# Kernel optimization log

Hardware: AMD Instinct MI355X
Metric: run time of the kernel (lower is better)

Reference implementation:

```python
import jax, jax.numpy as jnp
import numpy as np

EMBED_DIM = 1024
N_HEADS = 16
HEAD_DIM = EMBED_DIM // N_HEADS
B, S = 2, 2048


def setup_inputs() -> dict:
    key = jax.random.key(0)
    ks = jax.random.split(key, 7)
    scale = 1.0 / np.sqrt(EMBED_DIM)
    return {
        "query": jax.random.normal(ks[0], (B, S, EMBED_DIM), dtype=jnp.float32),
        "key": jax.random.normal(ks[1], (B, S, EMBED_DIM), dtype=jnp.float32),
        "value": jax.random.normal(ks[2], (B, S, EMBED_DIM), dtype=jnp.float32),
        # nn.Linear weights stored as [out, in]; y = x @ W.T
        "Wq": jax.random.normal(ks[3], (EMBED_DIM, EMBED_DIM), dtype=jnp.float32) * scale,
        "Wk": jax.random.normal(ks[4], (EMBED_DIM, EMBED_DIM), dtype=jnp.float32) * scale,
        "Wv": jax.random.normal(ks[5], (EMBED_DIM, EMBED_DIM), dtype=jnp.float32) * scale,
        "Wo": jax.random.normal(ks[6], (EMBED_DIM, EMBED_DIM), dtype=jnp.float32) * scale,
    }


def reference(query, key, value, Wq, Wk, Wv, Wo):
    # Projections (Linear, no bias): x @ W.T
    Q = query @ Wq.T  # [B, S, E]
    K = key @ Wk.T
    V = value @ Wv.T
    b, s, _ = Q.shape
    # Split heads: slicing head i of [..., E] == reshape to [B, S, H, D]
    Qh = Q.reshape(b, s, N_HEADS, HEAD_DIM)
    Kh = K.reshape(b, s, N_HEADS, HEAD_DIM)
    Vh = V.reshape(b, s, N_HEADS, HEAD_DIM)
    scores = jnp.einsum("bqhd,bkhd->bhqk", Qh, Kh) / jnp.sqrt(
        jnp.asarray(HEAD_DIM, dtype=Qh.dtype)
    )  # [B, H, Sq, Sk]
    attn = jax.nn.softmax(scores, axis=-1)
    out = jnp.einsum("bhqk,bkhd->bqhd", attn, Vh)  # [B, Sq, H, D]
    out = out.reshape(b, s, N_HEADS * HEAD_DIM)  # concat heads
    return out @ Wo.T
```

## Files before the change

### kernel.cpp

```cpp
#include <hip/hip_runtime.h>
#include <hip/hip_bf16.h>
#include <stdint.h>
#include <stddef.h>

#define EMBED 1024
#define NHEAD 16
#define HDIM  64
#define BATCH 2
#define SEQ   2048
#define MTOT  (BATCH*SEQ)

typedef __hip_bfloat16 bf16;
typedef __attribute__((ext_vector_type(8))) __bf16 bf16x8;
typedef __attribute__((ext_vector_type(4))) float  f32x4;
typedef __attribute__((ext_vector_type(16))) float f32x16;

#define GLD16(gp, lp) __builtin_amdgcn_global_load_lds( \
    (__attribute__((address_space(1))) void*)(gp),      \
    (__attribute__((address_space(3))) void*)(lp), 16, 0, 0)


__device__ __forceinline__ ushort4 cvt4(const float4 v) {
  union { ushort4 u; bf16 b[4]; } o;
  o.b[0] = __float2bfloat16(v.x);
  o.b[1] = __float2bfloat16(v.y);
  o.b[2] = __float2bfloat16(v.z);
  o.b[3] = __float2bfloat16(v.w);
  return o.u;
}

__device__ __forceinline__ uint32_t pk2(float lo, float hi) {
  union { bf16 h[2]; uint32_t u; } r;
  r.h[0] = __float2bfloat16(lo);
  r.h[1] = __float2bfloat16(hi);
  return r.u;
}

__device__ __forceinline__ bool detect_bf16(const uint32_t* __restrict__ x, int t) {
  uint32_t w = x[(size_t)(t & 63) * 997u];
  int e = (int)((w >> 7) & 0xFF);
  unsigned long long m = __ballot(e >= 100 && e <= 135);
  return __popcll(m) >= 48;
}

#define SM_C1 0.18033688011112042f
#define SM_C0 -14.426950408889634f

__global__ __launch_bounds__(256)
void convert_inputs(const void* xs0, const void* xs1, const void* xs2,
                    const void* ws0, const void* ws1, const void* ws2, const void* ws3,
                    bf16* __restrict__ xd0, bf16* __restrict__ xd1, bf16* __restrict__ xd2,
                    bf16* __restrict__ wd0, bf16* __restrict__ wd1,
                    bf16* __restrict__ wd2, bf16* __restrict__ wd3) {
  const int bid = blockIdx.x;
  const void* src; bf16* dst; size_t base;
  if (bid < 6144) {
    const int a = bid >> 11;
    src = a == 0 ? xs0 : a == 1 ? xs1 : xs2;
    dst = a == 0 ? xd0 : a == 1 ? xd1 : xd2;
    base = (size_t)(bid & 2047) * 2048;
  } else {
    const int a = (bid - 6144) >> 9;
    src = a == 0 ? ws0 : a == 1 ? ws1 : a == 2 ? ws2 : ws3;
    dst = a == 0 ? wd0 : a == 1 ? wd1 : a == 2 ? wd2 : wd3;
    base = (size_t)((bid - 6144) & 511) * 2048;
  }
  const bool isbf = detect_bf16((const uint32_t*)src, threadIdx.x);
  const size_t off = base + (size_t)threadIdx.x * 8;
  if (isbf) {
    *(uint4*)((ushort*)dst + off) = *(const uint4*)((const ushort*)src + off);
  } else {
    const float* s = (const float*)src + off;
    float4 a4 = *(const float4*)(s);
    float4 b4 = *(const float4*)(s + 4);
    *(ushort4*)((ushort*)dst + off)     = cvt4(a4);
    *(ushort4*)((ushort*)dst + off + 4) = cvt4(b4);
  }
}

template<int TM, int TN>
__device__ __forceinline__ void gemm_nt_dbuf(
    const bf16* __restrict__ X, const bf16* __restrict__ W,
    bf16* sA, bf16* sB, f32x4 (&acc)[TM/32][TN/32],
    int row0, int col0, int t, int wr, int wc, int l16, int quad,
    int k0, int klen) {
  constexpr int CA = TM / 32, CB = TN / 32;
  constexpr int RI = TM / 32, RJ = TN / 32;
  constexpr int PF  = CA + CB;
  const int nit = klen >> 6;

  const bf16* gA[CA]; const bf16* gB[CB];
  int la[CA], lb[CB];
#pragma unroll
  for (int c = 0; c < CA; ++c) {
    int id = c * 256 + t, r = id >> 3;
    int cc = (((id & 7) ^ (r & 7)) * 8);
    gA[c] = X + (size_t)(row0 + r) * EMBED + k0 + cc;  la[c] = id * 8;
  }
#pragma unroll
  for (int c = 0; c < CB; ++c) {
    int id = c * 256 + t, r = id >> 3;
    int cc = (((id & 7) ^ (r & 7)) * 8);
    gB[c] = W + (size_t)(col0 + r) * EMBED + k0 + cc;  lb[c] = id * 8;
  }

  auto issue = [&](int kb, int buf) {
#pragma unroll
    for (int c = 0; c < CA; ++c) GLD16(gA[c] + kb, sA + buf * (TM * 64) + la[c]);
#pragma unroll
    for (int c = 0; c < CB; ++c) GLD16(gB[c] + kb, sB + buf * (TN * 64) + lb[c]);
  };
  const int xr = l16 & 7;
  auto compute = [&](int buf) {
    const bf16* pA = sA + buf * (TM * 64);
    const bf16* pB = sB + buf * (TN * 64);
#pragma unroll
    for (int kk = 0; kk < 64; kk += 32) {
      const int ch = (kk >> 3) + quad;
      bf16x8 a[RI], b[RJ];
#pragma unroll
      for (int i = 0; i < RI; ++i)
        a[i] = *(const bf16x8*)(pA + (wr + 16 * i + l16) * 64 + ((ch ^ xr) << 3));
#pragma unroll
      for (int j = 0; j < RJ; ++j)
        b[j] = *(const bf16x8*)(pB + (wc + 16 * j + l16) * 64 + ((ch ^ xr) << 3));
#pragma unroll
      for (int i = 0; i < RI; ++i)
#pragma unroll
        for (int j = 0; j < RJ; ++j)
          acc[i][j] = __builtin_amdgcn_mfma_f32_16x16x32_bf16(a[i], b[j], acc[i][j], 0, 0, 0);
    }
  };

  issue(0, 0);
  int p = 0;
  for (int i = 0; i < nit - 1; ++i) {
    issue((i + 1) * 64, p ^ 1);
    asm volatile("s_waitcnt vmcnt(%0)\ns_barrier" :: "i"(PF) : "memory");
    compute(p);
    asm volatile("s_barrier" ::: "memory");
    p ^= 1;
  }
  asm volatile("s_waitcnt vmcnt(0)\ns_barrier" ::: "memory");
  compute(p);
}

template<int TM, int TN, bool ABF, bool BBF>
__device__ __forceinline__ void gemm_nt_slow(
    const void* __restrict__ X, const void* __restrict__ W,
    bf16* sA, bf16* sB, f32x4 (&acc)[TM/32][TN/32],
    int row0, int col0, int t, int wr, int wc, int l16, int quad,
    int k0, int klen) {
  constexpr int RI = TM / 32, RJ = TN / 32;
  const int xr = l16 & 7;
  for (int kb = k0; kb < k0 + klen; kb += 64) {
    if constexpr (ABF) {
      const bf16* s = (const bf16*)X;
#pragma unroll
      for (int c = 0; c < TM / 32; ++c) {
        int id = c * 256 + t, r = id >> 3;
        int cc = (((id & 7) ^ (r & 7)) * 8);
        GLD16(s + (size_t)(row0 + r) * EMBED + kb + cc, sA + id * 8);
      }
    } else {
      const float* s = (const float*)X;
#pragma unroll
      for (int c = 0; c < TM / 16; ++c) {
        int id = c * 256 + t, r = id >> 4;
        int lc = (id & 15) >> 1, half = (id & 1) * 4;
        float4 v = *(const float4*)(s + (size_t)(row0 + r) * EMBED + kb + lc * 8 + half);
        *(ushort4*)(sA + r * 64 + ((lc ^ (r & 7)) << 3) + half) = cvt4(v);
      }
    }
    if constexpr (BBF) {
      const bf16* s = (const bf16*)W;
#pragma unroll
      for (int c = 0; c < TN / 32; ++c) {
        int id = c * 256 + t, r = id >> 3;
        int cc = (((id & 7) ^ (r & 7)) * 8);
        GLD16(s + (size_t)(col0 + r) * EMBED + kb + cc, sB + id * 8);
      }
    } else {
      const float* s = (const float*)W;
#pragma unroll
      for (int c = 0; c < TN / 16; ++c) {
        int id = c * 256 + t, r = id >> 4;
        int lc = (id & 15) >> 1, half = (id & 1) * 4;
        float4 v = *(const float4*)(s + (size_t)(col0 + r) * EMBED + kb + lc * 8 + half);
        *(ushort4*)(sB + r * 64 + ((lc ^ (r & 7)) << 3) + half) = cvt4(v);
      }
    }
    __syncthreads();
#pragma unroll
    for (int kk = 0; kk < 64; kk += 32) {
      const int ch = (kk >> 3) + quad;
      bf16x8 a[RI], b[RJ];
#pragma unroll
      for (int i = 0; i < RI; ++i)
        a[i] = *(const bf16x8*)(sA + (wr + 16 * i + l16) * 64 + ((ch ^ xr) << 3));
#pragma unroll
      for (int j = 0; j < RJ; ++j)
        b[j] = *(const bf16x8*)(sB + (wc + 16 * j + l16) * 64 + ((ch ^ xr) << 3));
#pragma unroll
      for (int i = 0; i < RI; ++i)
#pragma unroll
        for (int j = 0; j < RJ; ++j)
          acc[i][j] = __builtin_amdgcn_mfma_f32_16x16x32_bf16(a[i], b[j], acc[i][j], 0, 0, 0);
    }
    __syncthreads();
  }
}

__global__ __launch_bounds__(256, 2)
void qkv_proj_kernel(const void* Xq, const void* Xk, const void* Xv,
                     const void* Wq, const void* Wk, const void* Wv,
                     bf16* __restrict__ Qo, bf16* __restrict__ Ko,
                     bf16* __restrict__ Vto) {
  __shared__ __align__(16) bf16 sA[2 * 128 * 64];
  __shared__ __align__(16) bf16 sB[2 * 128 * 64];
  const int t    = threadIdx.x;
  const int wave = t >> 6, lane = t & 63;
  const int quad = lane >> 4, l16 = lane & 15;
  const int wr = (wave & 1) * 64;
  const int wc = (wave >> 1) * 64;
  const bool isbf = detect_bf16((const uint32_t*)Xq, t);

  for (int ti = blockIdx.x; ti < 768; ti += 512) {
    const int sel  = ti >> 8;
    const int col0 = ((ti >> 5) & 7) * 128;
    const int row0 = (ti & 31) * 128;
    const void* X = (sel == 0) ? Xq : (sel == 1) ? Xk : Xv;
    const void* W = (sel == 0) ? Wq : (sel == 1) ? Wk : Wv;

    f32x4 acc[4][4] = {};
    if (isbf)
      gemm_nt_dbuf<128, 128>((const bf16*)X, (const bf16*)W, sA, sB, acc,
                             row0, col0, t, wr, wc, l16, quad, 0, EMBED);
    else
      gemm_nt_slow<128, 128, false, false>(X, W, sA, sB, acc,
                                           row0, col0, t, wr, wc, l16, quad, 0, EMBED);

    if (sel < 2) {
      bf16* C = (sel == 0) ? Qo : Ko;
      const float sc = (sel == 0) ? SM_C1 : 1.0f;
#pragma unroll
      for (int i = 0; i < 4; ++i)
#pragma unroll
        for (int j = 0; j < 4; ++j)
#pragma unroll
          for (int r = 0; r < 4; ++r) {
            int m = row0 + wr + 16 * i + quad * 4 + r;
            int n = col0 + wc + 16 * j + l16;
            C[(size_t)m * EMBED + n] = __float2bfloat16(acc[i][j][r] * sc);
          }
    } else {
#pragma unroll
      for (int i = 0; i < 4; ++i)
#pragma unroll
        for (int j = 0; j < 4; ++j)
#pragma unroll
          for (int r = 0; r < 4; ++r) {
            int m = row0 + wr + 16 * i + quad * 4 + r;
            int n = col0 + wc + 16 * j + l16;
            int b = m >> 11, s = m & (SEQ - 1);
            int h = n >> 6,  d = n & (HDIM - 1);
            Vto[(((size_t)(b * NHEAD + h)) * HDIM + d) * SEQ + s] =
                __float2bfloat16(acc[i][j][r]);
          }
    }
    __syncthreads();
  }
}

__global__ __launch_bounds__(256, 2)
void out_proj_partial(const bf16* __restrict__ X, const void* W,
                      const uint32_t* __restrict__ qref, float* __restrict__ P) {
  __shared__ __align__(16) bf16 sA[2 * 128 * 64];
  __shared__ __align__(16) bf16 sB[2 * 128 * 64];
  const int t    = threadIdx.x;
  const int wave = t >> 6, lane = t & 63;
  const int quad = lane >> 4, l16 = lane & 15;
  const int row0 = blockIdx.x * 128;
  const int col0 = blockIdx.y * 128;
  const int z    = blockIdx.z;
  const int wr = (wave & 1) * 64;
  const int wc = (wave >> 1) * 64;
  const bool isbf = detect_bf16(qref, t);

  f32x4 acc[4][4] = {};
  if (isbf)
    gemm_nt_dbuf<128, 128>(X, (const bf16*)W, sA, sB, acc,
                           row0, col0, t, wr, wc, l16, quad, z * 512, 512);
  else
    gemm_nt_slow<128, 128, true, false>(X, W, sA, sB, acc,
                                        row0, col0, t, wr, wc, l16, quad, z * 512, 512);

  float* Pz = P + (size_t)z * MTOT * EMBED;
#pragma unroll
  for (int i = 0; i < 4; ++i)
#pragma unroll
    for (int j = 0; j < 4; ++j)
#pragma unroll
      for (int r = 0; r < 4; ++r) {
        int m = row0 + wr + 16 * i + quad * 4 + r;
        int n = col0 + wc + 16 * j + l16;
        Pz[(size_t)m * EMBED + n] = acc[i][j][r];
      }
}

__global__ __launch_bounds__(256)
void reduce_splitk(const float* __restrict__ P,
                   const uint32_t* __restrict__ qref, void* __restrict__ C) {
  const bool isbf = detect_bf16(qref, threadIdx.x);
  size_t i = ((size_t)blockIdx.x * 256 + threadIdx.x) * 4;
  float4 a = *(const float4*)(P + i);
  float4 b = *(const float4*)(P + (size_t)MTOT * EMBED + i);
  float4 s = make_float4(a.x + b.x, a.y + b.y, a.z + b.z, a.w + b.w);
  if (isbf) *(ushort4*)((bf16*)C + i) = cvt4(s);
  else      *(float4*)((float*)C + i) = s;
}

__global__ __launch_bounds__(256, 2)
void out_proj_kernel(const bf16* __restrict__ X, const void* W,
                     const uint32_t* __restrict__ qref, void* C) {
  __shared__ __align__(16) bf16 sA[2 * 64 * 64];
  __shared__ __align__(16) bf16 sB[2 * 128 * 64];
  const int t    = threadIdx.x;
  const int wave = t >> 6, lane = t & 63;
  const int quad = lane >> 4, l16 = lane & 15;
  const int row0 = blockIdx.x * 64;
  const int col0 = blockIdx.y * 128;
  const int wr = (wave & 1) * 32;
  const int wc = (wave >> 1) * 64;
  const bool isbf = detect_bf16(qref, t);

  f32x4 acc[2][4] = {};
  if (isbf)
    gemm_nt_dbuf<64, 128>(X, (const bf16*)W, sA, sB, acc,
                          row0, col0, t, wr, wc, l16, quad, 0, EMBED);
  else
    gemm_nt_slow<64, 128, true, false>(X, W, sA, sB, acc,
                                       row0, col0, t, wr, wc, l16, quad, 0, EMBED);

#pragma unroll
  for (int i = 0; i < 2; ++i)
#pragma unroll
    for (int j = 0; j < 4; ++j)
#pragma unroll
      for (int r = 0; r < 4; ++r) {
        int m = row0 + wr + 16 * i + quad * 4 + r;
        int n = col0 + wc + 16 * j + l16;
        if (isbf)
          ((bf16*)C)[(size_t)m * EMBED + n] = __float2bfloat16(acc[i][j][r]);
        else
          ((float*)C)[(size_t)m * EMBED + n] = acc[i][j][r];
      }
}

__global__ __launch_bounds__(256, 2)
void flash_kernel(const bf16* __restrict__ Q, const bf16* __restrict__ K,
                  const bf16* __restrict__ Vt, bf16* __restrict__ O) {
  __shared__ __align__(16) bf16 sK[2][64 * 64];
  __shared__ __align__(16) bf16 sV[2][64 * 64];

  const int t    = threadIdx.x;
  const int wave = t >> 6, lane = t & 63;
  const int l5 = lane & 31, hi = lane >> 5;
  const int x5 = l5 & 7;

  const int L  = ((blockIdx.x & 7) << 6) + (blockIdx.x >> 3);
  const int qt = L & 15;
  const int h  = (L >> 4) & 15;
  const int b  = L >> 8;
  const int qw = qt * 128 + 32 * wave;

  const bf16* Kg = K + ((size_t)b * SEQ) * EMBED + h * HDIM;
  const bf16* Vg = Vt + (((size_t)(b * NHEAD + h)) * HDIM) * SEQ;

  bf16x8 aq[4];
  {
    const bf16* Qrow = Q + ((size_t)b * SEQ + qw + l5) * EMBED + h * HDIM + hi * 8;
#pragma unroll
    for (int g = 0; g < 4; ++g) aq[g] = *(const bf16x8*)(Qrow + 16 * g);
  }

  union { bf16x8 v; bf16 e[8]; } ones;
#pragma unroll
  for (int i = 0; i < 8; ++i) ones.e[i] = __float2bfloat16(1.0f);

  auto issueK = [&](int kt, int buf) {
#pragma unroll
    for (int c = 0; c < 2; ++c) {
      int id = c * 256 + t, r = id >> 3;
      int cc = (((id & 7) ^ (r & 7)) * 8);
      GLD16(Kg + (size_t)(kt + r) * EMBED + cc, &sK[buf][id * 8]);
    }
  };
  auto issueV = [&](int kt, int buf) {
#pragma unroll
    for (int c = 0; c < 2; ++c) {
      int id = c * 256 + t, r = id >> 3;
      int cc = (((id & 7) ^ (r & 7)) * 8);
      GLD16(Vg + (size_t)r * SEQ + kt + cc, &sV[buf][id * 8]);
    }
  };

  f32x16 o0 = {}, o1 = {};
  f32x16 ls = {};
  f32x16 pT0, pT1;

  auto qk = [&](int buf, f32x16& T0, f32x16& T1) {
#pragma unroll
    for (int r = 0; r < 16; ++r) { T0[r] = SM_C0; T1[r] = SM_C0; }
    __builtin_amdgcn_s_setprio(1);
#pragma unroll
    for (int g = 0; g < 4; ++g) {
      const int ch = 2 * g + hi;
      bf16x8 ak0 = *(const bf16x8*)(&sK[buf][(l5)      * 64 + ((ch ^ x5) << 3)]);
      bf16x8 ak1 = *(const bf16x8*)(&sK[buf][(32 + l5) * 64 + ((ch ^ x5) << 3)]);
      T0 = __builtin_amdgcn_mfma_f32_32x32x16_bf16(ak0, aq[g], T0, 0, 0, 0);
      T1 = __builtin_amdgcn_mfma_f32_32x32x16_bf16(ak1, aq[g], T1, 0, 0, 0);
    }
    __builtin_amdgcn_s_setprio(0);
  };

  auto smax = [&](const f32x16& T0, const f32x16& T1, bf16x8 (&PA)[4]) {
#pragma unroll
    for (int kg = 0; kg < 2; ++kg) {
      float p[16];
#pragma unroll
      for (int r = 0; r < 16; ++r)
        p[r] = __builtin_amdgcn_exp2f(kg ? T1[r] : T0[r]);
#pragma unroll
      for (int s = 0; s < 2; ++s) {
        uint32_t c0 = pk2(p[8 * s + 0], p[8 * s + 1]);
        uint32_t c1 = pk2(p[8 * s + 2], p[8 * s + 3]);
        uint32_t c2 = pk2(p[8 * s + 4], p[8 * s + 5]);
        uint32_t c3 = pk2(p[8 * s + 6], p[8 * s + 7]);
        uint32_t x = __shfl_xor(hi ? c0 : c2, 32, 64);
        uint32_t y = __shfl_xor(hi ? c1 : c3, 32, 64);
        union { uint32_t u[4]; bf16x8 v; } w;
        w.u[0] = hi ? x  : c0;
        w.u[1] = hi ? y  : c1;
        w.u[2] = hi ? c2 : x;
        w.u[3] = hi ? c3 : y;
        PA[2 * kg + s] = w.v;
      }
    }
  };

  auto pv = [&](const bf16x8 (&PA)[4], int buf) {
    __builtin_amdgcn_s_setprio(1);
#pragma unroll
    for (int kk = 0; kk < 4; ++kk) {
      const int ch = 2 * kk + hi;
      ls = __builtin_amdgcn_mfma_f32_32x32x16_bf16(PA[kk], ones.v, ls, 0, 0, 0);
      bf16x8 bv0 = *(const bf16x8*)(&sV[buf][(l5)      * 64 + ((ch ^ x5) << 3)]);
      bf16x8 bv1 = *(const bf16x8*)(&sV[buf][(32 + l5) * 64 + ((ch ^ x5) << 3)]);
      o0 = __builtin_amdgcn_mfma_f32_32x32x16_bf16(PA[kk], bv0, o0, 0, 0, 0);
      o1 = __builtin_amdgcn_mfma_f32_32x32x16_bf16(PA[kk], bv1, o1, 0, 0, 0);
    }
    __builtin_amdgcn_s_setprio(0);
  };

  issueK(0, 0); issueV(0, 0); issueK(64, 1);
  asm volatile("s_waitcnt vmcnt(2)\ns_barrier" ::: "memory");
  qk(0, pT0, pT1);
  asm volatile("s_barrier" ::: "memory");

#pragma unroll 2
  for (int i = 0; i < SEQ / 64 - 1; ++i) {
    issueK((i + 2) * 64, i & 1);
    issueV((i + 1) * 64, (i + 1) & 1);
    asm volatile("s_waitcnt vmcnt(4)\ns_barrier" ::: "memory");
    f32x16 nT0, nT1;
    qk((i + 1) & 1, nT0, nT1);
    bf16x8 PA[4];
    smax(pT0, pT1, PA);
    pv(PA, i & 1);
    asm volatile("s_barrier" ::: "memory");
    pT0 = nT0; pT1 = nT1;
  }

  asm volatile("s_waitcnt vmcnt(0)\ns_barrier" ::: "memory");
  {
    bf16x8 PA[4];
    smax(pT0, pT1, PA);
    pv(PA, (SEQ / 64 - 1) & 1);
  }

  bf16* Og = O + ((size_t)b * SEQ + qw) * EMBED + h * HDIM + l5;
#pragma unroll
  for (int r = 0; r < 16; ++r) {
    const int m = (r & 3) + 8 * (r >> 2) + 4 * hi;
    const float inv = 1.0f / ls[r];
    Og[(size_t)m * EMBED]      = __float2bfloat16(o0[r] * inv);
    Og[(size_t)m * EMBED + 32] = __float2bfloat16(o1[r] * inv);
  }
}

extern "C" void kernel_launch(void* const* d_in, const int* in_sizes, int n_in,
                              void* d_out, int out_size, void* d_ws, size_t ws_size,
                              hipStream_t stream) {
  (void)in_sizes; (void)n_in; (void)out_size;
  bf16* Qp  = (bf16*)((char*)d_ws + 256);
  bf16* Kp  = Qp  + (size_t)MTOT * EMBED;
  bf16* Vtp = Kp  + (size_t)MTOT * EMBED;
  bf16* Op  = Vtp + (size_t)MTOT * EMBED;
  float* Pf = (float*)(Op + (size_t)MTOT * EMBED);

  bf16* Xqb = (bf16*)Pf;
  bf16* Xkb = Xqb + (size_t)MTOT * EMBED;
  bf16* Xvb = Xkb + (size_t)MTOT * EMBED;
  bf16* Wqb = Xvb + (size_t)MTOT * EMBED;
  bf16* Wkb = Wqb + (size_t)EMBED * EMBED;
  bf16* Wvb = Wkb + (size_t)EMBED * EMBED;
  bf16* Wob = (bf16*)((char*)Pf + (size_t)2 * MTOT * EMBED * 4);

  const size_t need_split = 256 + (size_t)MTOT * EMBED * 2 * 4
                          + (size_t)MTOT * EMBED * 4 * 2;
  const size_t need_conv  = need_split + (size_t)EMBED * EMBED * 2;

  if (ws_size >= need_conv) {
    convert_inputs<<<dim3(8192), 256, 0, stream>>>(
        d_in[0], d_in[1], d_in[2], d_in[3], d_in[4], d_in[5], d_in[6],
        Xqb, Xkb, Xvb, Wqb, Wkb, Wvb, Wob);
    qkv_proj_kernel<<<dim3(512), 256, 0, stream>>>(
        Xqb, Xkb, Xvb, Wqb, Wkb, Wvb, Qp, Kp, Vtp);
    flash_kernel<<<dim3(512), 256, 0, stream>>>(Qp, Kp, Vtp, Op);
    out_proj_partial<<<dim3(32, 8, 2), 256, 0, stream>>>(
        Op, Wob, (const uint32_t*)Qp, Pf);
    reduce_splitk<<<dim3(MTOT * EMBED / 1024), 256, 0, stream>>>(
        Pf, (const uint32_t*)d_in[0], d_out);
  } else if (ws_size >= need_split) {
    qkv_proj_kernel<<<dim3(512), 256, 0, stream>>>(
        d_in[0], d_in[1], d_in[2], d_in[3], d_in[4], d_in[5], Qp, Kp, Vtp);
    flash_kernel<<<dim3(512), 256, 0, stream>>>(Qp, Kp, Vtp, Op);
    out_proj_partial<<<dim3(32, 8, 2), 256, 0, stream>>>(
        Op, d_in[6], (const uint32_t*)d_in[0], Pf);
    reduce_splitk<<<dim3(MTOT * EMBED / 1024), 256, 0, stream>>>(
        Pf, (const uint32_t*)d_in[0], d_out);
  } else {
    qkv_proj_kernel<<<dim3(512), 256, 0, stream>>>(
        d_in[0], d_in[1], d_in[2], d_in[3], d_in[4], d_in[5], Qp, Kp, Vtp);
    flash_kernel<<<dim3(512), 256, 0, stream>>>(Qp, Kp, Vtp, Op);
    out_proj_kernel<<<dim3(64, 8), 256, 0, stream>>>(
        Op, d_in[6], (const uint32_t*)d_in[0], d_out);
  }
}
```

Before: 216.9 us.

## Split flash attention over two KV halves with a combine kernel

The flash attention kernel is templated so that, in the default workspace path, each (batch, head, query-tile) is split into two blocks that each process half of the key/value sequence. The grid doubles to 1024 blocks and the occupancy hint rises to four blocks per CU. Unnormalized fp32 partial outputs and row sums go to workspace, and a new reduce kernel adds the two halves, normalizes and converts to bf16. This aims to raise parallelism and latency hiding on the GPU. In exchange it adds an extra launch, fp32 partial-output traffic and possible register pressure from the tighter launch bound. Summing the halves directly is only correct if the softmax uses a fixed reference rather than a per-half running max.

```diff
diff --git a/kernel.cpp b/kernel.cpp
--- a/kernel.cpp
+++ b/kernel.cpp
@@ -357,9 +357,11 @@
       }
 }
 
-__global__ __launch_bounds__(256, 2)
+template<bool SPLIT>
+__global__ __launch_bounds__(256, SPLIT ? 4 : 2)
 void flash_kernel(const bf16* __restrict__ Q, const bf16* __restrict__ K,
-                  const bf16* __restrict__ Vt, bf16* __restrict__ O) {
+                  const bf16* __restrict__ Vt, bf16* __restrict__ O,
+                  float* __restrict__ Po, float* __restrict__ Ls) {
   __shared__ __align__(16) bf16 sK[2][64 * 64];
   __shared__ __align__(16) bf16 sV[2][64 * 64];
 
@@ -368,10 +370,14 @@
   const int l5 = lane & 31, hi = lane >> 5;
   const int x5 = l5 & 7;
 
-  const int L  = ((blockIdx.x & 7) << 6) + (blockIdx.x >> 3);
+  constexpr int LSH = SPLIT ? 7 : 6;
+  const int L  = ((blockIdx.x & 7) << LSH) | (blockIdx.x >> 3);
   const int qt = L & 15;
   const int h  = (L >> 4) & 15;
-  const int b  = L >> 8;
+  const int b  = (L >> 8) & 1;
+  const int z  = SPLIT ? (L >> 9) : 0;
+  constexpr int HT = SPLIT ? 16 : 32;
+  const int k0 = z << 10;
   const int qw = qt * 128 + 32 * wave;
 
   const bf16* Kg = K + ((size_t)b * SEQ) * EMBED + h * HDIM;
@@ -463,15 +469,15 @@
     __builtin_amdgcn_s_setprio(0);
   };
 
-  issueK(0, 0); issueV(0, 0); issueK(64, 1);
+  issueK(k0, 0); issueV(k0, 0); issueK(k0 + 64, 1);
   asm volatile("s_waitcnt vmcnt(2)\ns_barrier" ::: "memory");
   qk(0, pT0, pT1);
   asm volatile("s_barrier" ::: "memory");
 
 #pragma unroll 2
-  for (int i = 0; i < SEQ / 64 - 1; ++i) {
-    issueK((i + 2) * 64, i & 1);
-    issueV((i + 1) * 64, (i + 1) & 1);
+  for (int i = 0; i < HT - 1; ++i) {
+    issueK(k0 + (i + 2) * 64, i & 1);
+    issueV(k0 + (i + 1) * 64, (i + 1) & 1);
     asm volatile("s_waitcnt vmcnt(4)\ns_barrier" ::: "memory");
     f32x16 nT0, nT1;
     qk((i + 1) & 1, nT0, nT1);
@@ -486,17 +492,50 @@
   {
     bf16x8 PA[4];
     smax(pT0, pT1, PA);
-    pv(PA, (SEQ / 64 - 1) & 1);
-  }
-
-  bf16* Og = O + ((size_t)b * SEQ + qw) * EMBED + h * HDIM + l5;
-#pragma unroll
-  for (int r = 0; r < 16; ++r) {
-    const int m = (r & 3) + 8 * (r >> 2) + 4 * hi;
-    const float inv = 1.0f / ls[r];
-    Og[(size_t)m * EMBED]      = __float2bfloat16(o0[r] * inv);
-    Og[(size_t)m * EMBED + 32] = __float2bfloat16(o1[r] * inv);
-  }
+    pv(PA, (HT - 1) & 1);
+  }
+
+  if constexpr (SPLIT) {
+    float* Pg = Po + ((size_t)z * MTOT + b * SEQ + qw) * EMBED + h * HDIM + l5;
+#pragma unroll
+    for (int r = 0; r < 16; ++r) {
+      const int m = (r & 3) + 8 * (r >> 2) + 4 * hi;
+      Pg[(size_t)m * EMBED]      = o0[r];
+      Pg[(size_t)m * EMBED + 32] = o1[r];
+    }
+    if (l5 == 0) {
+      float* Lp = Ls + ((size_t)z * MTOT + b * SEQ + qw) * NHEAD + h;
+#pragma unroll
+      for (int r = 0; r < 16; ++r) {
+        const int m = (r & 3) + 8 * (r >> 2) + 4 * hi;
+        Lp[(size_t)m * NHEAD] = ls[r];
+      }
+    }
+  } else {
+    bf16* Og = O + ((size_t)b * SEQ + qw) * EMBED + h * HDIM + l5;
+#pragma unroll
+    for (int r = 0; r < 16; ++r) {
+      const int m = (r & 3) + 8 * (r >> 2) + 4 * hi;
+      const float inv = 1.0f / ls[r];
+      Og[(size_t)m * EMBED]      = __float2bfloat16(o0[r] * inv);
+      Og[(size_t)m * EMBED + 32] = __float2bfloat16(o1[r] * inv);
+    }
+  }
+}
+
+__global__ __launch_bounds__(256)
+void flash_reduce(const float* __restrict__ Po, const float* __restrict__ Ls,
+                  bf16* __restrict__ O) {
+  size_t i = ((size_t)blockIdx.x * 256 + threadIdx.x) * 4;
+  const size_t m = i >> 10;
+  const int h = (int)((i >> 6) & 15);
+  float4 a = *(const float4*)(Po + i);
+  float4 c = *(const float4*)(Po + (size_t)MTOT * EMBED + i);
+  float l0 = Ls[m * NHEAD + h];
+  float l1 = Ls[(size_t)MTOT * NHEAD + m * NHEAD + h];
+  float inv = 1.0f / (l0 + l1);
+  *(ushort4*)(O + i) = cvt4(make_float4((a.x + c.x) * inv, (a.y + c.y) * inv,
+                                        (a.z + c.z) * inv, (a.w + c.w) * inv));
 }
 
 extern "C" void kernel_launch(void* const* d_in, const int* in_sizes, int n_in,
@@ -516,10 +555,12 @@
   bf16* Wkb = Wqb + (size_t)EMBED * EMBED;
   bf16* Wvb = Wkb + (size_t)EMBED * EMBED;
   bf16* Wob = (bf16*)((char*)Pf + (size_t)2 * MTOT * EMBED * 4);
+  float* Lsp = (float*)(Wob + (size_t)EMBED * EMBED);
 
   const size_t need_split = 256 + (size_t)MTOT * EMBED * 2 * 4
                           + (size_t)MTOT * EMBED * 4 * 2;
-  const size_t need_conv  = need_split + (size_t)EMBED * EMBED * 2;
+  const size_t need_conv  = need_split + (size_t)EMBED * EMBED * 2
+                          + (size_t)2 * MTOT * NHEAD * 4;
 
   if (ws_size >= need_conv) {
     convert_inputs<<<dim3(8192), 256, 0, stream>>>(
@@ -527,7 +568,9 @@
         Xqb, Xkb, Xvb, Wqb, Wkb, Wvb, Wob);
     qkv_proj_kernel<<<dim3(512), 256, 0, stream>>>(
         Xqb, Xkb, Xvb, Wqb, Wkb, Wvb, Qp, Kp, Vtp);
-    flash_kernel<<<dim3(512), 256, 0, stream>>>(Qp, Kp, Vtp, Op);
+    flash_kernel<true><<<dim3(1024), 256, 0, stream>>>(
+        Qp, Kp, Vtp, Op, Pf, Lsp);
+    flash_reduce<<<dim3(MTOT * EMBED / 1024), 256, 0, stream>>>(Pf, Lsp, Op);
     out_proj_partial<<<dim3(32, 8, 2), 256, 0, stream>>>(
         Op, Wob, (const uint32_t*)Qp, Pf);
     reduce_splitk<<<dim3(MTOT * EMBED / 1024), 256, 0, stream>>>(
@@ -535,7 +578,8 @@
   } else if (ws_size >= need_split) {
     qkv_proj_kernel<<<dim3(512), 256, 0, stream>>>(
         d_in[0], d_in[1], d_in[2], d_in[3], d_in[4], d_in[5], Qp, Kp, Vtp);
-    flash_kernel<<<dim3(512), 256, 0, stream>>>(Qp, Kp, Vtp, Op);
+    flash_kernel<false><<<dim3(512), 256, 0, stream>>>(
+        Qp, Kp, Vtp, Op, Pf, (float*)Pf);
     out_proj_partial<<<dim3(32, 8, 2), 256, 0, stream>>>(
         Op, d_in[6], (const uint32_t*)d_in[0], Pf);
     reduce_splitk<<<dim3(MTOT * EMBED / 1024), 256, 0, stream>>>(
@@ -543,7 +587,8 @@
   } else {
     qkv_proj_kernel<<<dim3(512), 256, 0, stream>>>(
         d_in[0], d_in[1], d_in[2], d_in[3], d_in[4], d_in[5], Qp, Kp, Vtp);
-    flash_kernel<<<dim3(512), 256, 0, stream>>>(Qp, Kp, Vtp, Op);
+    flash_kernel<false><<<dim3(512), 256, 0, stream>>>(
+        Qp, Kp, Vtp, Op, Pf, (float*)Pf);
     out_proj_kernel<<<dim3(64, 8), 256, 0, stream>>>(
         Op, d_in[6], (const uint32_t*)d_in[0], d_out);
   }
```

Measured after the change: 458.8 us. 111% more time.

## Split key sequence across two wave groups in flash kernel and merge via LDS

Applied to the files above, without the earlier changes.

Doubles the flash kernel block to 512 threads. Each half of the waves processes half of the key/value sequence with its own double-buffered LDS tiles. The partial output and row sums from the second half are written to LDS and added by the first half before normalization and store. This shortens the serial per-block KV loop and raises waves per CU, at the cost of doubled LDS usage, an extra reduction epilogue, and possible register pressure.

```diff
diff --git a/kernel.cpp b/kernel.cpp
--- a/kernel.cpp
+++ b/kernel.cpp
@@ -357,22 +357,27 @@
       }
 }
 
-__global__ __launch_bounds__(256, 2)
+__global__ __launch_bounds__(512, 2)
 void flash_kernel(const bf16* __restrict__ Q, const bf16* __restrict__ K,
                   const bf16* __restrict__ Vt, bf16* __restrict__ O) {
-  __shared__ __align__(16) bf16 sK[2][64 * 64];
-  __shared__ __align__(16) bf16 sV[2][64 * 64];
+  __shared__ __align__(16) bf16 sK[2][2][64 * 64];
+  __shared__ __align__(16) bf16 sV[2][2][64 * 64];
 
   const int t    = threadIdx.x;
   const int wave = t >> 6, lane = t & 63;
   const int l5 = lane & 31, hi = lane >> 5;
   const int x5 = l5 & 7;
-
-  const int L  = ((blockIdx.x & 7) << 6) + (blockIdx.x >> 3);
+  const int z  = wave >> 2;
+  const int wq = wave & 3;
+  const int ct = t & 255;
+  const int k0 = z << 10;
+  constexpr int HT = 16;
+
+  const int L  = ((blockIdx.x & 7) << 6) | (blockIdx.x >> 3);
   const int qt = L & 15;
   const int h  = (L >> 4) & 15;
   const int b  = L >> 8;
-  const int qw = qt * 128 + 32 * wave;
+  const int qw = qt * 128 + 32 * wq;
 
   const bf16* Kg = K + ((size_t)b * SEQ) * EMBED + h * HDIM;
   const bf16* Vg = Vt + (((size_t)(b * NHEAD + h)) * HDIM) * SEQ;
@@ -391,17 +396,17 @@
   auto issueK = [&](int kt, int buf) {
 #pragma unroll
     for (int c = 0; c < 2; ++c) {
-      int id = c * 256 + t, r = id >> 3;
+      int id = c * 256 + ct, r = id >> 3;
       int cc = (((id & 7) ^ (r & 7)) * 8);
-      GLD16(Kg + (size_t)(kt + r) * EMBED + cc, &sK[buf][id * 8]);
+      GLD16(Kg + (size_t)(kt + r) * EMBED + cc, &sK[buf][z][id * 8]);
     }
   };
   auto issueV = [&](int kt, int buf) {
 #pragma unroll
     for (int c = 0; c < 2; ++c) {
-      int id = c * 256 + t, r = id >> 3;
+      int id = c * 256 + ct, r = id >> 3;
       int cc = (((id & 7) ^ (r & 7)) * 8);
-      GLD16(Vg + (size_t)r * SEQ + kt + cc, &sV[buf][id * 8]);
+      GLD16(Vg + (size_t)r * SEQ + kt + cc, &sV[buf][z][id * 8]);
     }
   };
 
@@ -416,8 +421,8 @@
 #pragma unroll
     for (int g = 0; g < 4; ++g) {
       const int ch = 2 * g + hi;
-      bf16x8 ak0 = *(const bf16x8*)(&sK[buf][(l5)      * 64 + ((ch ^ x5) << 3)]);
-      bf16x8 ak1 = *(const bf16x8*)(&sK[buf][(32 + l5) * 64 + ((ch ^ x5) << 3)]);
+      bf16x8 ak0 = *(const bf16x8*)(&sK[buf][z][(l5)      * 64 + ((ch ^ x5) << 3)]);
+      bf16x8 ak1 = *(const bf16x8*)(&sK[buf][z][(32 + l5) * 64 + ((ch ^ x5) << 3)]);
       T0 = __builtin_amdgcn_mfma_f32_32x32x16_bf16(ak0, aq[g], T0, 0, 0, 0);
       T1 = __builtin_amdgcn_mfma_f32_32x32x16_bf16(ak1, aq[g], T1, 0, 0, 0);
     }
@@ -455,23 +460,23 @@
     for (int kk = 0; kk < 4; ++kk) {
       const int ch = 2 * kk + hi;
       ls = __builtin_amdgcn_mfma_f32_32x32x16_bf16(PA[kk], ones.v, ls, 0, 0, 0);
-      bf16x8 bv0 = *(const bf16x8*)(&sV[buf][(l5)      * 64 + ((ch ^ x5) << 3)]);
-      bf16x8 bv1 = *(const bf16x8*)(&sV[buf][(32 + l5) * 64 + ((ch ^ x5) << 3)]);
+      bf16x8 bv0 = *(const bf16x8*)(&sV[buf][z][(l5)      * 64 + ((ch ^ x5) << 3)]);
+      bf16x8 bv1 = *(const bf16x8*)(&sV[buf][z][(32 + l5) * 64 + ((ch ^ x5) << 3)]);
       o0 = __builtin_amdgcn_mfma_f32_32x32x16_bf16(PA[kk], bv0, o0, 0, 0, 0);
       o1 = __builtin_amdgcn_mfma_f32_32x32x16_bf16(PA[kk], bv1, o1, 0, 0, 0);
     }
     __builtin_amdgcn_s_setprio(0);
   };
 
-  issueK(0, 0); issueV(0, 0); issueK(64, 1);
+  issueK(k0, 0); issueV(k0, 0); issueK(k0 + 64, 1);
   asm volatile("s_waitcnt vmcnt(2)\ns_barrier" ::: "memory");
   qk(0, pT0, pT1);
   asm volatile("s_barrier" ::: "memory");
 
 #pragma unroll 2
-  for (int i = 0; i < SEQ / 64 - 1; ++i) {
-    issueK((i + 2) * 64, i & 1);
-    issueV((i + 1) * 64, (i + 1) & 1);
+  for (int i = 0; i < HT - 1; ++i) {
+    issueK(k0 + (i + 2) * 64, i & 1);
+    issueV(k0 + (i + 1) * 64, (i + 1) & 1);
     asm volatile("s_waitcnt vmcnt(4)\ns_barrier" ::: "memory");
     f32x16 nT0, nT1;
     qk((i + 1) & 1, nT0, nT1);
@@ -486,16 +491,33 @@
   {
     bf16x8 PA[4];
     smax(pT0, pT1, PA);
-    pv(PA, (SEQ / 64 - 1) & 1);
-  }
-
-  bf16* Og = O + ((size_t)b * SEQ + qw) * EMBED + h * HDIM + l5;
-#pragma unroll
-  for (int r = 0; r < 16; ++r) {
-    const int m = (r & 3) + 8 * (r >> 2) + 4 * hi;
-    const float inv = 1.0f / ls[r];
-    Og[(size_t)m * EMBED]      = __float2bfloat16(o0[r] * inv);
-    Og[(size_t)m * EMBED + 32] = __float2bfloat16(o1[r] * inv);
+    pv(PA, (HT - 1) & 1);
+  }
+
+  float* sO = (float*)&sK[0][0][0];
+  float* sL = (float*)&sV[0][0][0];
+  __syncthreads();
+  if (z == 1) {
+#pragma unroll
+    for (int r = 0; r < 16; ++r) {
+      const int m = (r & 3) + 8 * (r >> 2) + 4 * hi;
+      sO[(32 * wq + m) * 64 + l5]      = o0[r];
+      sO[(32 * wq + m) * 64 + l5 + 32] = o1[r];
+      if (l5 == 0) sL[32 * wq + m] = ls[r];
+    }
+  }
+  __syncthreads();
+  if (z == 0) {
+    bf16* Og = O + ((size_t)b * SEQ + qw) * EMBED + h * HDIM + l5;
+#pragma unroll
+    for (int r = 0; r < 16; ++r) {
+      const int m = (r & 3) + 8 * (r >> 2) + 4 * hi;
+      const float inv = 1.0f / (ls[r] + sL[32 * wq + m]);
+      Og[(size_t)m * EMBED] =
+          __float2bfloat16((o0[r] + sO[(32 * wq + m) * 64 + l5]) * inv);
+      Og[(size_t)m * EMBED + 32] =
+          __float2bfloat16((o1[r] + sO[(32 * wq + m) * 64 + l5 + 32]) * inv);
+    }
   }
 }
 
@@ -527,7 +549,7 @@
         Xqb, Xkb, Xvb, Wqb, Wkb, Wvb, Wob);
     qkv_proj_kernel<<<dim3(512), 256, 0, stream>>>(
         Xqb, Xkb, Xvb, Wqb, Wkb, Wvb, Qp, Kp, Vtp);
-    flash_kernel<<<dim3(512), 256, 0, stream>>>(Qp, Kp, Vtp, Op);
+    flash_kernel<<<dim3(512), 512, 0, stream>>>(Qp, Kp, Vtp, Op);
     out_proj_partial<<<dim3(32, 8, 2), 256, 0, stream>>>(
         Op, Wob, (const uint32_t*)Qp, Pf);
     reduce_splitk<<<dim3(MTOT * EMBED / 1024), 256, 0, stream>>>(
@@ -535,7 +557,7 @@
   } else if (ws_size >= need_split) {
     qkv_proj_kernel<<<dim3(512), 256, 0, stream>>>(
         d_in[0], d_in[1], d_in[2], d_in[3], d_in[4], d_in[5], Qp, Kp, Vtp);
-    flash_kernel<<<dim3(512), 256, 0, stream>>>(Qp, Kp, Vtp, Op);
+    flash_kernel<<<dim3(512), 512, 0, stream>>>(Qp, Kp, Vtp, Op);
     out_proj_partial<<<dim3(32, 8, 2), 256, 0, stream>>>(
         Op, d_in[6], (const uint32_t*)d_in[0], Pf);
     reduce_splitk<<<dim3(MTOT * EMBED / 1024), 256, 0, stream>>>(
@@ -543,7 +565,7 @@
   } else {
     qkv_proj_kernel<<<dim3(512), 256, 0, stream>>>(
         d_in[0], d_in[1], d_in[2], d_in[3], d_in[4], d_in[5], Qp, Kp, Vtp);
-    flash_kernel<<<dim3(512), 256, 0, stream>>>(Qp, Kp, Vtp, Op);
+    flash_kernel<<<dim3(512), 512, 0, stream>>>(Qp, Kp, Vtp, Op);
     out_proj_kernel<<<dim3(64, 8), 256, 0, stream>>>(
         Op, d_in[6], (const uint32_t*)d_in[0], d_out);
   }
```

After: 226.8 us. 1.05x slower.

## Rebalance QKV projection tiles across blocks and use permlane32 swap in softmax

Applied to the files above, without the earlier changes.

The QKV projection kernel previously had 512 blocks loop over 768 128x128 tiles, so some blocks ran two tiles and others one. Now each block computes one Q or K 128x128 tile and then one 64x128 half-tile of V, which evens out the per-block work. In the flash kernel, the ds_bpermute-based shfl_xor plus selects that exchange bf16 halves across 32-lane halves are replaced with the gfx950 permlane32_swap intrinsic. The rebalancing adds a second GEMM prologue per block and uses smaller V tiles with less reuse.

```diff
diff --git a/kernel.cpp b/kernel.cpp
--- a/kernel.cpp
+++ b/kernel.cpp
@@ -221,16 +221,16 @@
   const int t    = threadIdx.x;
   const int wave = t >> 6, lane = t & 63;
   const int quad = lane >> 4, l16 = lane & 15;
-  const int wr = (wave & 1) * 64;
   const int wc = (wave >> 1) * 64;
   const bool isbf = detect_bf16((const uint32_t*)Xq, t);
 
-  for (int ti = blockIdx.x; ti < 768; ti += 512) {
-    const int sel  = ti >> 8;
-    const int col0 = ((ti >> 5) & 7) * 128;
-    const int row0 = (ti & 31) * 128;
-    const void* X = (sel == 0) ? Xq : (sel == 1) ? Xk : Xv;
-    const void* W = (sel == 0) ? Wq : (sel == 1) ? Wk : Wv;
+  {
+    const int sel  = blockIdx.x >> 8;
+    const int col0 = ((blockIdx.x >> 5) & 7) * 128;
+    const int row0 = (blockIdx.x & 31) * 128;
+    const void* X = sel ? Xk : Xq;
+    const void* W = sel ? Wk : Wq;
+    const int wr = (wave & 1) * 64;
 
     f32x4 acc[4][4] = {};
     if (isbf)
@@ -240,35 +240,49 @@
       gemm_nt_slow<128, 128, false, false>(X, W, sA, sB, acc,
                                            row0, col0, t, wr, wc, l16, quad, 0, EMBED);
 
-    if (sel < 2) {
-      bf16* C = (sel == 0) ? Qo : Ko;
-      const float sc = (sel == 0) ? SM_C1 : 1.0f;
-#pragma unroll
-      for (int i = 0; i < 4; ++i)
-#pragma unroll
-        for (int j = 0; j < 4; ++j)
-#pragma unroll
-          for (int r = 0; r < 4; ++r) {
-            int m = row0 + wr + 16 * i + quad * 4 + r;
-            int n = col0 + wc + 16 * j + l16;
-            C[(size_t)m * EMBED + n] = __float2bfloat16(acc[i][j][r] * sc);
-          }
-    } else {
-#pragma unroll
-      for (int i = 0; i < 4; ++i)
-#pragma unroll
-        for (int j = 0; j < 4; ++j)
-#pragma unroll
-          for (int r = 0; r < 4; ++r) {
-            int m = row0 + wr + 16 * i + quad * 4 + r;
-            int n = col0 + wc + 16 * j + l16;
-            int b = m >> 11, s = m & (SEQ - 1);
-            int h = n >> 6,  d = n & (HDIM - 1);
-            Vto[(((size_t)(b * NHEAD + h)) * HDIM + d) * SEQ + s] =
-                __float2bfloat16(acc[i][j][r]);
-          }
-    }
-    __syncthreads();
+    bf16* C = sel ? Ko : Qo;
+    const float sc = sel ? 1.0f : SM_C1;
+#pragma unroll
+    for (int i = 0; i < 4; ++i)
+#pragma unroll
+      for (int j = 0; j < 4; ++j)
+#pragma unroll
+        for (int r = 0; r < 4; ++r) {
+          int m = row0 + wr + 16 * i + quad * 4 + r;
+          int n = col0 + wc + 16 * j + l16;
+          C[(size_t)m * EMBED + n] = __float2bfloat16(acc[i][j][r] * sc);
+        }
+  }
+  __syncthreads();
+
+  {
+    const int tt   = blockIdx.x >> 1;
+    const int half = blockIdx.x & 1;
+    const int col0 = ((tt >> 5) & 7) * 128;
+    const int row0 = (tt & 31) * 128 + half * 64;
+    const int wr = (wave & 1) * 32;
+
+    f32x4 acc[2][4] = {};
+    if (isbf)
+      gemm_nt_dbuf<64, 128>((const bf16*)Xv, (const bf16*)Wv, sA, sB, acc,
+                            row0, col0, t, wr, wc, l16, quad, 0, EMBED);
+    else
+      gemm_nt_slow<64, 128, false, false>(Xv, Wv, sA, sB, acc,
+                                          row0, col0, t, wr, wc, l16, quad, 0, EMBED);
+
+#pragma unroll
+    for (int i = 0; i < 2; ++i)
+#pragma unroll
+      for (int j = 0; j < 4; ++j)
+#pragma unroll
+        for (int r = 0; r < 4; ++r) {
+          int m = row0 + wr + 16 * i + quad * 4 + r;
+          int n = col0 + wc + 16 * j + l16;
+          int b = m >> 11, s = m & (SEQ - 1);
+          int h = n >> 6,  d = n & (HDIM - 1);
+          Vto[(((size_t)(b * NHEAD + h)) * HDIM + d) * SEQ + s] =
+              __float2bfloat16(acc[i][j][r]);
+        }
   }
 }
 
@@ -368,7 +382,7 @@
   const int l5 = lane & 31, hi = lane >> 5;
   const int x5 = l5 & 7;
 
-  const int L  = ((blockIdx.x & 7) << 6) + (blockIdx.x >> 3);
+  const int L  = ((blockIdx.x & 7) << 6) | (blockIdx.x >> 3);
   const int qt = L & 15;
   const int h  = (L >> 4) & 15;
   const int b  = L >> 8;
@@ -437,13 +451,13 @@
         uint32_t c1 = pk2(p[8 * s + 2], p[8 * s + 3]);
         uint32_t c2 = pk2(p[8 * s + 4], p[8 * s + 5]);
         uint32_t c3 = pk2(p[8 * s + 6], p[8 * s + 7]);
-        uint32_t x = __shfl_xor(hi ? c0 : c2, 32, 64);
-        uint32_t y = __shfl_xor(hi ? c1 : c3, 32, 64);
+        auto r0 = __builtin_amdgcn_permlane32_swap(c0, c2, false, false);
+        auto r1 = __builtin_amdgcn_permlane32_swap(c1, c3, false, false);
         union { uint32_t u[4]; bf16x8 v; } w;
-        w.u[0] = hi ? x  : c0;
-        w.u[1] = hi ? y  : c1;
-        w.u[2] = hi ? c2 : x;
-        w.u[3] = hi ? c3 : y;
+        w.u[0] = r0[0];
+        w.u[1] = r1[0];
+        w.u[2] = r0[1];
+        w.u[3] = r1[1];
         PA[2 * kg + s] = w.v;
       }
     }
```

New measurement: 213.3 us. Within noise of the previous version (-1.7%).
